# Optimization experiments

Hardware: AMD Instinct MI355X
Metric: run time of the kernel (lower is better)

## Reference

```python
import jax, jax.numpy as jnp
import numpy as np

TNEI = 2
TOPK = 4
NEIGH = 2 * TNEI + 1  # window size = 5


def _normalize(x, eps=1e-12):
    # matches torch F.normalize(dim=-1)
    n = jnp.linalg.norm(x, axis=-1, keepdims=True)
    return x / jnp.maximum(n, eps)


def setup_inputs() -> dict:
    key = jax.random.key(0)
    ks = jax.random.split(key, 10)
    B, T, C = 32, 256, 128
    x = jax.random.normal(ks[0], (B, T, C), jnp.float32)
    radj = jax.random.randint(ks[1], (B, T, T), 0, 2).astype(jnp.int32)
    inxs = jax.random.randint(ks[2], (B, T, TOPK), 0, T)
    s = 1.0 / np.sqrt(C)
    W_pf = jax.random.normal(ks[3], (C, C), jnp.float32) * s
    W_ns = jax.random.normal(ks[4], (C, C), jnp.float32) * s
    W_v = jax.random.normal(ks[5], (C, C), jnp.float32) * s
    v_pf = jax.random.normal(ks[6], (NEIGH,), jnp.float32)
    g_pf = jnp.linalg.norm(v_pf)[None]  # weight_norm gain, shape (1,)
    v_ns = jax.random.normal(ks[7], (TOPK,), jnp.float32)
    g_ns = jnp.linalg.norm(v_ns)[None]
    return dict(x=x, radj=radj, inxs=inxs, W_pf=W_pf, W_ns=W_ns, W_v=W_v,
                v_pf=v_pf, g_pf=g_pf, v_ns=v_ns, g_ns=g_ns)


def reference(x, radj, inxs, W_pf, W_ns, W_v, v_pf, g_pf, v_ns, g_ns):
    B, T, C = x.shape
    pf = _normalize(x @ W_pf.T)
    ns = _normalize(x @ W_ns.T)
    v = x @ W_v.T
    # windowed neighbor indices, identical to _tneigh_mask(mode='all')
    i = jnp.arange(T)
    start = jnp.clip(i - TNEI, 0, T - NEIGH)
    nbr = start[:, None] + jnp.arange(NEIGH)[None, :]  # (T, NEIGH)
    ctx = pf[:, nbr]  # (B, T, NEIGH, C) — replaces one-hot ctxinx einsum
    # pairwise window similarity: (B,T,T,n,n)
    sim = jnp.einsum('bxic,byjc->bxyij', ctx, ctx)
    # AdaptiveMaxPool2d((n,1)) == max over the last (key-window) axis
    sim_pf = sim.max(axis=-1)  # (B,T,T,n)
    w_pf = g_pf[0] * v_pf / jnp.linalg.norm(v_pf)  # weight-norm agg_pf
    sim_pf = jnp.einsum('bxyi,i->bxy', sim_pf, w_pf)
    # topk-neighbor branch: inxs gathers ns rows (replaces one-hot einsum)
    ns_q = ns[jnp.arange(B)[:, None, None], inxs]  # (B,T,TOPK,C)
    sim_ns = jnp.einsum('bxnc,byc->bxyn', ns_q, ns)  # (B,T,T,TOPK)
    w_ns = g_ns[0] * v_ns / jnp.linalg.norm(v_ns)  # weight-norm agg_ns
    sim_ns = jnp.einsum('bxyn,n->bxy', sim_ns, w_ns)
    # adjacency mask: 0 -> -1e22, >0 -> 0
    mask = jnp.where(radj == 0, jnp.float32(-1e22), jnp.float32(0.0))
    attn = jax.nn.softmax(sim_pf + sim_ns + mask, axis=-1)  # (B,T,T)
    return jnp.einsum('bkt,btd->bkd', attn, v)  # (B,T,C)
```

## Files before the change

### kernel.cpp

```cpp
#include <hip/hip_runtime.h>
#include <math.h>


#define TT 256
#define CC 128

using bf16x8 = __attribute__((ext_vector_type(8))) short;
using f32x4  = __attribute__((ext_vector_type(4))) float;

__device__ __forceinline__ short bf_hi(float x) {
    unsigned u = __float_as_uint(x);
    return (short)((u + 0x7FFFu + ((u >> 16) & 1u)) >> 16);
}
__device__ __forceinline__ void bf_split(float x, short& h, short& l) {
    h = bf_hi(x);
    float hf = __uint_as_float(((unsigned)(unsigned short)h) << 16);
    l = bf_hi(x - hf);
}
__device__ __forceinline__ float max5(float a, float b, float c, float d, float e) {
    return fmaxf(fmaxf(fmaxf(a, b), fmaxf(c, d)), e);
}

__global__ __launch_bounds__(256) void proj_kernel(
    const float* __restrict__ x,
    const float* __restrict__ W0, const float* __restrict__ W1, const float* __restrict__ W2,
    short* __restrict__ pf_h, short* __restrict__ pf_l,
    short* __restrict__ ns_h, short* __restrict__ ns_l,
    float* __restrict__ ns_f, float* __restrict__ v_f)
{
    __shared__ float xs[64][36];
    __shared__ float Ws[128][36];
    const int tid = threadIdx.x, ty = tid >> 4, tx = tid & 15;
    const int row0 = blockIdx.x * 64;
    const int m = blockIdx.y;
    const float* __restrict__ W = (m == 0) ? W0 : (m == 1) ? W1 : W2;
    float acc[4][8] = {};

    for (int k0 = 0; k0 < CC; k0 += 32) {
        __syncthreads();
        for (int i = 0; i < 2; i++) {
            int flat = i * 256 + tid, r = flat >> 3, q = (flat & 7) * 4;
            *(float4*)&xs[r][q] = *(const float4*)&x[(row0 + r) * CC + k0 + q];
        }
        for (int i = 0; i < 4; i++) {
            int flat = i * 256 + tid, r = flat >> 3, q = (flat & 7) * 4;
            *(float4*)&Ws[r][q] = *(const float4*)&W[r * CC + k0 + q];
        }
        __syncthreads();
        for (int kq = 0; kq < 32; kq += 4) {
            float4 av[4], bv[8];
            for (int u = 0; u < 4; u++) av[u] = *(float4*)&xs[ty + 16 * u][kq];
            for (int w = 0; w < 8; w++) bv[w] = *(float4*)&Ws[tx + 16 * w][kq];
            for (int u = 0; u < 4; u++)
                for (int w = 0; w < 8; w++) {
                    acc[u][w] = fmaf(av[u].x, bv[w].x, acc[u][w]);
                    acc[u][w] = fmaf(av[u].y, bv[w].y, acc[u][w]);
                    acc[u][w] = fmaf(av[u].z, bv[w].z, acc[u][w]);
                    acc[u][w] = fmaf(av[u].w, bv[w].w, acc[u][w]);
                }
        }
    }
    for (int u = 0; u < 4; u++) {
        int row = row0 + ty + 16 * u;
        if (m == 2) {
            for (int w = 0; w < 8; w++) v_f[row * CC + tx + 16 * w] = acc[u][w];
        } else {
            float ss = 0.f;
            for (int w = 0; w < 8; w++) ss += acc[u][w] * acc[u][w];
            for (int off = 8; off; off >>= 1) ss += __shfl_xor(ss, off);
            float inv = 1.f / fmaxf(sqrtf(ss), 1e-12f);
            for (int w = 0; w < 8; w++) {
                float v = acc[u][w] * inv;
                short h, l;
                bf_split(v, h, l);
                int idx = row * CC + tx + 16 * w;
                if (m == 0) { pf_h[idx] = h; pf_l[idx] = l; }
                else        { ns_h[idx] = h; ns_l[idx] = l; ns_f[idx] = v; }
            }
        }
    }
}

__global__ __launch_bounds__(256) void prep_kernel(
    const float* __restrict__ ns_f, const int* __restrict__ inxs,
    const float* __restrict__ v_ns, const float* __restrict__ g_ns,
    const float* __restrict__ v_f,
    short* __restrict__ q_h, short* __restrict__ q_l,
    short* __restrict__ vt_h, short* __restrict__ vt_l)
{
    __shared__ float Ls[64][132];
    const int bx = blockIdx.x, tid = threadIdx.x;
    if (bx < 512) {
        float n2 = v_ns[0]*v_ns[0] + v_ns[1]*v_ns[1] + v_ns[2]*v_ns[2] + v_ns[3]*v_ns[3];
        float sc = g_ns[0] / sqrtf(n2);
        const float w0 = sc*v_ns[0], w1 = sc*v_ns[1], w2 = sc*v_ns[2], w3 = sc*v_ns[3];
        for (int it = 0; it < 2; it++) {
            int t4 = bx * 512 + it * 256 + tid;
            int q = (t4 & 31) * 4, gr = t4 >> 5;
            int b = gr >> 8;
            int4 id = *(const int4*)&inxs[gr * 4];
            const float* Nb = ns_f + (size_t)b * TT * CC;
            float4 aa = *(const float4*)&Nb[id.x * CC + q];
            float4 ab = *(const float4*)&Nb[id.y * CC + q];
            float4 ac = *(const float4*)&Nb[id.z * CC + q];
            float4 ad = *(const float4*)&Nb[id.w * CC + q];
            float4 r4;
            r4.x = w0*aa.x + w1*ab.x + w2*ac.x + w3*ad.x;
            r4.y = w0*aa.y + w1*ab.y + w2*ac.y + w3*ad.y;
            r4.z = w0*aa.z + w1*ab.z + w2*ac.z + w3*ad.z;
            r4.w = w0*aa.w + w1*ab.w + w2*ac.w + w3*ad.w;
            short4 h4, l4;
            bf_split(r4.x, h4.x, l4.x); bf_split(r4.y, h4.y, l4.y);
            bf_split(r4.z, h4.z, l4.z); bf_split(r4.w, h4.w, l4.w);
            *(short4*)&q_h[(size_t)gr * CC + q] = h4;
            *(short4*)&q_l[(size_t)gr * CC + q] = l4;
        }
    } else {
        int blk = bx - 512;
        int b = blk >> 2, t0 = (blk & 3) * 64;
        const float* Vb = v_f + (size_t)b * TT * CC;
        for (int i = 0; i < 8; i++) {
            int flat = i * 256 + tid, r = flat >> 5, cq = (flat & 31) * 4;
            *(float4*)&Ls[r][cq] = *(const float4*)&Vb[(t0 + r) * CC + cq];
        }
        __syncthreads();
        int c = tid & 127, th = tid >> 7;
        for (int j = 0; j < 8; j++) {
            short4 h4, l4;
            for (int e = 0; e < 4; e++) {
                float v = Ls[th * 32 + j * 4 + e][c];
                bf_split(v, ((short*)&h4)[e], ((short*)&l4)[e]);
            }
            size_t o = ((size_t)b * CC + c) * TT + t0 + th * 32 + j * 4;
            *(short4*)&vt_h[o] = h4;
            *(short4*)&vt_l[o] = l4;
        }
    }
}

__global__ __launch_bounds__(256) void gram_mfma(
    const short* __restrict__ pf_h, const short* __restrict__ pf_l,
    const short* __restrict__ ns_h, const short* __restrict__ ns_l,
    const short* __restrict__ q_h,  const short* __restrict__ q_l,
    float* __restrict__ G, float* __restrict__ S)
{
    const int tid = threadIdx.x;
    const int m0 = blockIdx.x * 64, n0 = blockIdx.y * 64;
    const int b = blockIdx.z >> 1, half = blockIdx.z & 1;
    const size_t base = (size_t)b * TT * CC;
    const short* __restrict__ Ahp = (half ? q_h : pf_h) + base;
    const short* __restrict__ Alp = (half ? q_l : pf_l) + base;
    const short* __restrict__ Bhp = (half ? ns_h : pf_h) + base;
    const short* __restrict__ Blp = (half ? ns_l : pf_l) + base;
    const int lane = tid & 63, wave = tid >> 6;
    const int wm = wave >> 1, wn = wave & 1;
    const int quad = lane >> 4, lr = lane & 15;
    const int am0 = (m0 + 32 * wm + lr) * CC, am1 = am0 + 16 * CC;
    const int bn0 = (n0 + 32 * wn + lr) * CC, bn1 = bn0 + 16 * CC;
    f32x4 z4 = {0.f, 0.f, 0.f, 0.f};
    f32x4 acc[2][2] = {{z4, z4}, {z4, z4}};
    #pragma unroll
    for (int k0 = 0; k0 < CC; k0 += 32) {
        int ko = k0 + quad * 8;
        bf16x8 a0h = *(const bf16x8*)&Ahp[am0 + ko];
        bf16x8 a0l = *(const bf16x8*)&Alp[am0 + ko];
        bf16x8 a1h = *(const bf16x8*)&Ahp[am1 + ko];
        bf16x8 a1l = *(const bf16x8*)&Alp[am1 + ko];
        bf16x8 b0h = *(const bf16x8*)&Bhp[bn0 + ko];
        bf16x8 b0l = *(const bf16x8*)&Blp[bn0 + ko];
        bf16x8 b1h = *(const bf16x8*)&Bhp[bn1 + ko];
        bf16x8 b1l = *(const bf16x8*)&Blp[bn1 + ko];
        acc[0][0] = __builtin_amdgcn_mfma_f32_16x16x32_bf16(a0h, b0h, acc[0][0], 0, 0, 0);
        acc[0][0] = __builtin_amdgcn_mfma_f32_16x16x32_bf16(a0h, b0l, acc[0][0], 0, 0, 0);
        acc[0][0] = __builtin_amdgcn_mfma_f32_16x16x32_bf16(a0l, b0h, acc[0][0], 0, 0, 0);
        acc[0][1] = __builtin_amdgcn_mfma_f32_16x16x32_bf16(a0h, b1h, acc[0][1], 0, 0, 0);
        acc[0][1] = __builtin_amdgcn_mfma_f32_16x16x32_bf16(a0h, b1l, acc[0][1], 0, 0, 0);
        acc[0][1] = __builtin_amdgcn_mfma_f32_16x16x32_bf16(a0l, b1h, acc[0][1], 0, 0, 0);
        acc[1][0] = __builtin_amdgcn_mfma_f32_16x16x32_bf16(a1h, b0h, acc[1][0], 0, 0, 0);
        acc[1][0] = __builtin_amdgcn_mfma_f32_16x16x32_bf16(a1h, b0l, acc[1][0], 0, 0, 0);
        acc[1][0] = __builtin_amdgcn_mfma_f32_16x16x32_bf16(a1l, b0h, acc[1][0], 0, 0, 0);
        acc[1][1] = __builtin_amdgcn_mfma_f32_16x16x32_bf16(a1h, b1h, acc[1][1], 0, 0, 0);
        acc[1][1] = __builtin_amdgcn_mfma_f32_16x16x32_bf16(a1h, b1l, acc[1][1], 0, 0, 0);
        acc[1][1] = __builtin_amdgcn_mfma_f32_16x16x32_bf16(a1l, b1h, acc[1][1], 0, 0, 0);
    }
    float* __restrict__ Cb = (half ? S : G) + (size_t)b * TT * TT;
    for (int tm = 0; tm < 2; tm++)
        for (int tn = 0; tn < 2; tn++) {
            int rb = m0 + 32 * wm + 16 * tm + quad * 4;
            int cb = n0 + 32 * wn + 16 * tn + lr;
            for (int reg = 0; reg < 4; reg++)
                Cb[(size_t)(rb + reg) * TT + cb] = acc[tm][tn][reg];
        }
}

__global__ __launch_bounds__(256, 2) void fused_smax_pv(
    const float* __restrict__ G, const float* __restrict__ S,
    const int* __restrict__ radj, const float* __restrict__ v_pf,
    const float* __restrict__ g_pf,
    const short* __restrict__ vt_h, const short* __restrict__ vt_l,
    float* __restrict__ out)
{
    __shared__ float Gs[20 * 256];
    __shared__ float RM[20 * 256];
    __shared__ short ATH[16 * 264];
    __shared__ short ATL[16 * 264];
    __shared__ float RD[64];
    __shared__ float RMX[64];
    const int tid = threadIdx.x;
    const int xt = blockIdx.x, b = blockIdx.y;
    const int x0 = xt * 16;
    const int rbase = min(max(x0 - 2, 0), TT - 5);
    for (int i = 0; i < 5; i++) {
        int flat = i * 256 + tid, ri = flat >> 6, q = (flat & 63) * 4;
        int r = min(rbase + ri, TT - 1);
        *(float4*)&Gs[ri * 256 + q] = *(const float4*)&G[(size_t)b * TT * TT + r * TT + q];
    }
    float n2 = 0.f;
    for (int i = 0; i < 5; i++) n2 += v_pf[i] * v_pf[i];
    float sc = g_pf[0] / sqrtf(n2);
    float wpf[5];
    for (int i = 0; i < 5; i++) wpf[i] = sc * v_pf[i];
    __syncthreads();
    for (int t = 0; t < 5; t++) {
        int task = t * 256 + tid;
        int i = task >> 6, g = task & 63;
        const float* row = &Gs[i * 256];
        float4 X = *(float4*)&row[4 * g];
        float m0_, m1_, m2_, m3_;
        if (g == 0) {
            float4 N = *(float4*)&row[4];
            float mx = fmaxf(fmaxf(X.x, X.y), fmaxf(X.z, X.w));
            m0_ = m1_ = m2_ = fmaxf(mx, N.x);
            m3_ = max5(X.y, X.z, X.w, N.x, N.y);
        } else if (g == 63) {
            float4 P = *(float4*)&row[248];
            m0_ = max5(P.z, P.w, X.x, X.y, X.z);
            float mx = fmaxf(fmaxf(X.x, X.y), fmaxf(X.z, X.w));
            m1_ = m2_ = m3_ = fmaxf(P.w, mx);
        } else {
            float4 P = *(float4*)&row[4 * g - 4];
            float4 N = *(float4*)&row[4 * g + 4];
            m0_ = max5(P.z, P.w, X.x, X.y, X.z);
            m1_ = max5(P.w, X.x, X.y, X.z, X.w);
            m2_ = max5(X.x, X.y, X.z, X.w, N.x);
            m3_ = max5(X.y, X.z, X.w, N.x, N.y);
        }
        float4 o4 = {m0_, m1_, m2_, m3_};
        *(float4*)&RM[i * 256 + 4 * g] = o4;
    }
    __syncthreads();
    const int y = tid;
    const size_t sb = (size_t)b * TT * TT;
    float lv[16];
    if (xt > 0 && xt < 15) {
        float rm[20];
        #pragma unroll
        for (int r = 0; r < 20; r++) rm[r] = RM[r * 256 + y];
        #pragma unroll
        for (int xi = 0; xi < 16; xi++) {
            float s = wpf[0] * rm[xi];
            #pragma unroll
            for (int i = 1; i < 5; i++) s = fmaf(wpf[i], rm[xi + i], s);
            lv[xi] = s;
        }
    } else {
        for (int xi = 0; xi < 16; xi++) {
            int sxr = min(max(x0 + xi - 2, 0), TT - 5) - rbase;
            float s = 0.f;
            for (int i = 0; i < 5; i++) s = fmaf(wpf[i], RM[(sxr + i) * 256 + y], s);
            lv[xi] = s;
        }
    }
    for (int xi = 0; xi < 16; xi++) {
        lv[xi] += S[sb + (x0 + xi) * TT + y];
        if (radj[sb + (x0 + xi) * TT + y] == 0) lv[xi] += -1e22f;
    }
    const int lane = tid & 63, wv = tid >> 6;
    for (int xi = 0; xi < 16; xi++) {
        float v = lv[xi];
        for (int o = 32; o; o >>= 1) v = fmaxf(v, __shfl_xor(v, o));
        if (lane == 0) RMX[xi * 4 + wv] = v;
    }
    __syncthreads();
    for (int xi = 0; xi < 16; xi++) {
        float mx = fmaxf(fmaxf(RMX[xi * 4], RMX[xi * 4 + 1]),
                         fmaxf(RMX[xi * 4 + 2], RMX[xi * 4 + 3]));
        float e = __expf(lv[xi] - mx);
        short h, l;
        bf_split(e, h, l);
        ATH[xi * 264 + y] = h;
        ATL[xi * 264 + y] = l;
        for (int o = 32; o; o >>= 1) e += __shfl_xor(e, o);
        if (lane == 0) RD[xi * 4 + wv] = e;
    }
    __syncthreads();
    const int quad = lane >> 4, lr = lane & 15;
    const int c0 = wv * 32;
    const short* __restrict__ vhb = vt_h + (size_t)b * CC * TT;
    const short* __restrict__ vlb = vt_l + (size_t)b * CC * TT;
    const int ar0 = (c0 + lr) * TT, ar1 = ar0 + 16 * TT;
    f32x4 z4 = {0.f, 0.f, 0.f, 0.f};
    f32x4 acc[2] = {z4, z4};
    #pragma unroll
    for (int k0 = 0; k0 < TT; k0 += 32) {
        int ko = k0 + quad * 8;
        bf16x8 bh = *(bf16x8*)&ATH[lr * 264 + ko];
        bf16x8 bl = *(bf16x8*)&ATL[lr * 264 + ko];
        bf16x8 a0h = *(const bf16x8*)&vhb[ar0 + ko];
        bf16x8 a0l = *(const bf16x8*)&vlb[ar0 + ko];
        bf16x8 a1h = *(const bf16x8*)&vhb[ar1 + ko];
        bf16x8 a1l = *(const bf16x8*)&vlb[ar1 + ko];
        acc[0] = __builtin_amdgcn_mfma_f32_16x16x32_bf16(a0h, bh, acc[0], 0, 0, 0);
        acc[0] = __builtin_amdgcn_mfma_f32_16x16x32_bf16(a0h, bl, acc[0], 0, 0, 0);
        acc[0] = __builtin_amdgcn_mfma_f32_16x16x32_bf16(a0l, bh, acc[0], 0, 0, 0);
        acc[1] = __builtin_amdgcn_mfma_f32_16x16x32_bf16(a1h, bh, acc[1], 0, 0, 0);
        acc[1] = __builtin_amdgcn_mfma_f32_16x16x32_bf16(a1h, bl, acc[1], 0, 0, 0);
        acc[1] = __builtin_amdgcn_mfma_f32_16x16x32_bf16(a1l, bh, acc[1], 0, 0, 0);
    }
    float sm = RD[lr * 4] + RD[lr * 4 + 1] + RD[lr * 4 + 2] + RD[lr * 4 + 3];
    float rinv = 1.f / sm;
    for (int tm = 0; tm < 2; tm++) {
        float4 r;
        r.x = acc[tm][0] * rinv; r.y = acc[tm][1] * rinv;
        r.z = acc[tm][2] * rinv; r.w = acc[tm][3] * rinv;
        *(float4*)&out[(size_t)b * TT * CC + (x0 + lr) * CC + c0 + 16 * tm + quad * 4] = r;
    }
}

extern "C" void kernel_launch(void* const* d_in, const int* in_sizes, int n_in,
                              void* d_out, int out_size, void* d_ws, size_t ws_size,
                              hipStream_t stream) {
    const float* x    = (const float*)d_in[0];
    const int*   radj = (const int*)d_in[1];
    const int*   inxs = (const int*)d_in[2];
    const float* Wpf  = (const float*)d_in[3];
    const float* Wns  = (const float*)d_in[4];
    const float* Wv   = (const float*)d_in[5];
    const float* v_pf = (const float*)d_in[6];
    const float* g_pf = (const float*)d_in[7];
    const float* v_ns = (const float*)d_in[8];
    const float* g_ns = (const float*)d_in[9];
    float* out = (float*)d_out;

    char* base = (char*)d_ws;
    float* ns_f = (float*)(base);
    float* v_f  = (float*)(base + (4u << 20));
    short* pf_h = (short*)(base + (8u << 20));
    short* pf_l = (short*)(base + (10u << 20));
    short* ns_h = (short*)(base + (12u << 20));
    short* ns_l = (short*)(base + (14u << 20));
    short* q_h  = (short*)(base + (16u << 20));
    short* q_l  = (short*)(base + (18u << 20));
    short* vt_h = (short*)(base + (20u << 20));
    short* vt_l = (short*)(base + (22u << 20));
    float* G    = (float*)(base + (24u << 20));
    float* S    = (float*)(base + (32u << 20));

    proj_kernel<<<dim3(128, 3), 256, 0, stream>>>(x, Wpf, Wns, Wv,
                                                  pf_h, pf_l, ns_h, ns_l, ns_f, v_f);
    prep_kernel<<<640, 256, 0, stream>>>(ns_f, inxs, v_ns, g_ns, v_f,
                                         q_h, q_l, vt_h, vt_l);
    gram_mfma<<<dim3(4, 4, 64), 256, 0, stream>>>(pf_h, pf_l, ns_h, ns_l, q_h, q_l, G, S);
    fused_smax_pv<<<dim3(16, 32), 256, 0, stream>>>(G, S, radj, v_pf, g_pf,
                                                    vt_h, vt_l, out);
}
```

Baseline: 144.5 us.

## Fuse prep into projection and gram kernels, use split-bf16 MFMA projections

The projection GEMM moves from scalar FP32 FMAs to split-bf16 (hi/lo) MFMA on 32-row tiles, and writes the transposed split V directly from the accumulators. The separate prep kernel is removed: the top-k weighted gather of ns rows now happens inside the gram kernel's shared-memory tile load, which also does the bf16 splitting on the fly from FP32 pf/ns. This removes one kernel launch and the intermediate hi/lo buffers. In exchange, the gram kernel does redundant gather and split work across column tiles, with extra LDS traffic and barriers.

```diff
diff --git a/kernel.cpp b/kernel.cpp
--- a/kernel.cpp
+++ b/kernel.cpp
@@ -21,167 +21,175 @@
     return fmaxf(fmaxf(fmaxf(a, b), fmaxf(c, d)), e);
 }
 
-__global__ __launch_bounds__(256) void proj_kernel(
+__global__ __launch_bounds__(256, 4) void proj_kernel(
     const float* __restrict__ x,
     const float* __restrict__ W0, const float* __restrict__ W1, const float* __restrict__ W2,
-    short* __restrict__ pf_h, short* __restrict__ pf_l,
-    short* __restrict__ ns_h, short* __restrict__ ns_l,
-    float* __restrict__ ns_f, float* __restrict__ v_f)
+    float* __restrict__ pf, float* __restrict__ ns,
+    short* __restrict__ vt_h, short* __restrict__ vt_l)
 {
-    __shared__ float xs[64][36];
-    __shared__ float Ws[128][36];
-    const int tid = threadIdx.x, ty = tid >> 4, tx = tid & 15;
-    const int row0 = blockIdx.x * 64;
+    __shared__ short Ah[32 * 40], Al[32 * 40];
+    __shared__ short Bh[128 * 40], Bl[128 * 40];
+    __shared__ float ssb[32][4];
+    const int tid = threadIdx.x;
+    const int row0 = blockIdx.x * 32;
     const int m = blockIdx.y;
     const float* __restrict__ W = (m == 0) ? W0 : (m == 1) ? W1 : W2;
-    float acc[4][8] = {};
+    const int lane = tid & 63, wn = tid >> 6;
+    const int quad = lane >> 4, lr = lane & 15;
+    f32x4 z4 = {0.f, 0.f, 0.f, 0.f};
+    f32x4 acc[2][2] = {{z4, z4}, {z4, z4}};
 
     for (int k0 = 0; k0 < CC; k0 += 32) {
         __syncthreads();
-        for (int i = 0; i < 2; i++) {
-            int flat = i * 256 + tid, r = flat >> 3, q = (flat & 7) * 4;
-            *(float4*)&xs[r][q] = *(const float4*)&x[(row0 + r) * CC + k0 + q];
+        {
+            int r = tid >> 3, q = (tid & 7) * 4;
+            float4 a4 = *(const float4*)&x[(row0 + r) * CC + k0 + q];
+            short4 h4, l4;
+            bf_split(a4.x, h4.x, l4.x); bf_split(a4.y, h4.y, l4.y);
+            bf_split(a4.z, h4.z, l4.z); bf_split(a4.w, h4.w, l4.w);
+            *(short4*)&Ah[r * 40 + q] = h4; *(short4*)&Al[r * 40 + q] = l4;
         }
         for (int i = 0; i < 4; i++) {
             int flat = i * 256 + tid, r = flat >> 3, q = (flat & 7) * 4;
-            *(float4*)&Ws[r][q] = *(const float4*)&W[r * CC + k0 + q];
-        }
-        __syncthreads();
-        for (int kq = 0; kq < 32; kq += 4) {
-            float4 av[4], bv[8];
-            for (int u = 0; u < 4; u++) av[u] = *(float4*)&xs[ty + 16 * u][kq];
-            for (int w = 0; w < 8; w++) bv[w] = *(float4*)&Ws[tx + 16 * w][kq];
-            for (int u = 0; u < 4; u++)
-                for (int w = 0; w < 8; w++) {
-                    acc[u][w] = fmaf(av[u].x, bv[w].x, acc[u][w]);
-                    acc[u][w] = fmaf(av[u].y, bv[w].y, acc[u][w]);
-                    acc[u][w] = fmaf(av[u].z, bv[w].z, acc[u][w]);
-                    acc[u][w] = fmaf(av[u].w, bv[w].w, acc[u][w]);
-                }
-        }
-    }
-    for (int u = 0; u < 4; u++) {
-        int row = row0 + ty + 16 * u;
-        if (m == 2) {
-            for (int w = 0; w < 8; w++) v_f[row * CC + tx + 16 * w] = acc[u][w];
-        } else {
-            float ss = 0.f;
-            for (int w = 0; w < 8; w++) ss += acc[u][w] * acc[u][w];
-            for (int off = 8; off; off >>= 1) ss += __shfl_xor(ss, off);
-            float inv = 1.f / fmaxf(sqrtf(ss), 1e-12f);
-            for (int w = 0; w < 8; w++) {
-                float v = acc[u][w] * inv;
-                short h, l;
-                bf_split(v, h, l);
-                int idx = row * CC + tx + 16 * w;
-                if (m == 0) { pf_h[idx] = h; pf_l[idx] = l; }
-                else        { ns_h[idx] = h; ns_l[idx] = l; ns_f[idx] = v; }
-            }
-        }
-    }
-}
-
-__global__ __launch_bounds__(256) void prep_kernel(
-    const float* __restrict__ ns_f, const int* __restrict__ inxs,
-    const float* __restrict__ v_ns, const float* __restrict__ g_ns,
-    const float* __restrict__ v_f,
-    short* __restrict__ q_h, short* __restrict__ q_l,
-    short* __restrict__ vt_h, short* __restrict__ vt_l)
+            float4 b4 = *(const float4*)&W[r * CC + k0 + q];
+            short4 h4, l4;
+            bf_split(b4.x, h4.x, l4.x); bf_split(b4.y, h4.y, l4.y);
+            bf_split(b4.z, h4.z, l4.z); bf_split(b4.w, h4.w, l4.w);
+            *(short4*)&Bh[r * 40 + q] = h4; *(short4*)&Bl[r * 40 + q] = l4;
+        }
+        __syncthreads();
+        bf16x8 ah[2], al[2], bh[2], bl[2];
+        for (int ra = 0; ra < 2; ra++) {
+            int ar = (16 * ra + lr) * 40 + quad * 8;
+            ah[ra] = *(bf16x8*)&Ah[ar];
+            al[ra] = *(bf16x8*)&Al[ar];
+        }
+        for (int tn = 0; tn < 2; tn++) {
+            int br = (32 * wn + 16 * tn + lr) * 40 + quad * 8;
+            bh[tn] = *(bf16x8*)&Bh[br];
+            bl[tn] = *(bf16x8*)&Bl[br];
+        }
+        for (int ra = 0; ra < 2; ra++)
+            for (int tn = 0; tn < 2; tn++) {
+                acc[ra][tn] = __builtin_amdgcn_mfma_f32_16x16x32_bf16(ah[ra], bh[tn], acc[ra][tn], 0, 0, 0);
+                acc[ra][tn] = __builtin_amdgcn_mfma_f32_16x16x32_bf16(ah[ra], bl[tn], acc[ra][tn], 0, 0, 0);
+                acc[ra][tn] = __builtin_amdgcn_mfma_f32_16x16x32_bf16(al[ra], bh[tn], acc[ra][tn], 0, 0, 0);
+            }
+    }
+    if (m < 2) {
+        float* __restrict__ o = (m == 0) ? pf : ns;
+        float ssp[2][4];
+        for (int ra = 0; ra < 2; ra++)
+            for (int reg = 0; reg < 4; reg++) {
+                float s = acc[ra][0][reg] * acc[ra][0][reg]
+                        + acc[ra][1][reg] * acc[ra][1][reg];
+                for (int off = 1; off < 16; off <<= 1) s += __shfl_xor(s, off);
+                ssp[ra][reg] = s;
+            }
+        if (lr == 0)
+            for (int ra = 0; ra < 2; ra++)
+                for (int reg = 0; reg < 4; reg++)
+                    ssb[16 * ra + quad * 4 + reg][wn] = ssp[ra][reg];
+        __syncthreads();
+        for (int ra = 0; ra < 2; ra++)
+            for (int reg = 0; reg < 4; reg++) {
+                int ml = 16 * ra + quad * 4 + reg;
+                float ss = ssb[ml][0] + ssb[ml][1] + ssb[ml][2] + ssb[ml][3];
+                float inv = 1.f / fmaxf(sqrtf(ss), 1e-12f);
+                int row = row0 + ml;
+                for (int tn = 0; tn < 2; tn++)
+                    o[row * CC + 32 * wn + 16 * tn + lr] = acc[ra][tn][reg] * inv;
+            }
+    } else {
+        for (int ra = 0; ra < 2; ra++) {
+            int rowbase = row0 + 16 * ra + quad * 4;
+            int b = rowbase >> 8, t0 = rowbase & 255;
+            for (int tn = 0; tn < 2; tn++) {
+                int c = 32 * wn + 16 * tn + lr;
+                short4 h4, l4;
+                for (int reg = 0; reg < 4; reg++)
+                    bf_split(acc[ra][tn][reg], ((short*)&h4)[reg], ((short*)&l4)[reg]);
+                size_t o = ((size_t)b * CC + c) * TT + t0;
+                *(short4*)&vt_h[o] = h4;
+                *(short4*)&vt_l[o] = l4;
+            }
+        }
+    }
+}
+
+__global__ __launch_bounds__(256, 4) void gram_mfma(
+    const float* __restrict__ pf, const float* __restrict__ ns,
+    const int* __restrict__ inxs, const float* __restrict__ v_ns,
+    const float* __restrict__ g_ns, float* __restrict__ G, float* __restrict__ S)
 {
-    __shared__ float Ls[64][132];
-    const int bx = blockIdx.x, tid = threadIdx.x;
-    if (bx < 512) {
-        float n2 = v_ns[0]*v_ns[0] + v_ns[1]*v_ns[1] + v_ns[2]*v_ns[2] + v_ns[3]*v_ns[3];
-        float sc = g_ns[0] / sqrtf(n2);
-        const float w0 = sc*v_ns[0], w1 = sc*v_ns[1], w2 = sc*v_ns[2], w3 = sc*v_ns[3];
-        for (int it = 0; it < 2; it++) {
-            int t4 = bx * 512 + it * 256 + tid;
-            int q = (t4 & 31) * 4, gr = t4 >> 5;
-            int b = gr >> 8;
-            int4 id = *(const int4*)&inxs[gr * 4];
-            const float* Nb = ns_f + (size_t)b * TT * CC;
-            float4 aa = *(const float4*)&Nb[id.x * CC + q];
-            float4 ab = *(const float4*)&Nb[id.y * CC + q];
-            float4 ac = *(const float4*)&Nb[id.z * CC + q];
-            float4 ad = *(const float4*)&Nb[id.w * CC + q];
-            float4 r4;
-            r4.x = w0*aa.x + w1*ab.x + w2*ac.x + w3*ad.x;
-            r4.y = w0*aa.y + w1*ab.y + w2*ac.y + w3*ad.y;
-            r4.z = w0*aa.z + w1*ab.z + w2*ac.z + w3*ad.z;
-            r4.w = w0*aa.w + w1*ab.w + w2*ac.w + w3*ad.w;
-            short4 h4, l4;
-            bf_split(r4.x, h4.x, l4.x); bf_split(r4.y, h4.y, l4.y);
-            bf_split(r4.z, h4.z, l4.z); bf_split(r4.w, h4.w, l4.w);
-            *(short4*)&q_h[(size_t)gr * CC + q] = h4;
-            *(short4*)&q_l[(size_t)gr * CC + q] = l4;
-        }
-    } else {
-        int blk = bx - 512;
-        int b = blk >> 2, t0 = (blk & 3) * 64;
-        const float* Vb = v_f + (size_t)b * TT * CC;
-        for (int i = 0; i < 8; i++) {
-            int flat = i * 256 + tid, r = flat >> 5, cq = (flat & 31) * 4;
-            *(float4*)&Ls[r][cq] = *(const float4*)&Vb[(t0 + r) * CC + cq];
-        }
-        __syncthreads();
-        int c = tid & 127, th = tid >> 7;
-        for (int j = 0; j < 8; j++) {
-            short4 h4, l4;
-            for (int e = 0; e < 4; e++) {
-                float v = Ls[th * 32 + j * 4 + e][c];
-                bf_split(v, ((short*)&h4)[e], ((short*)&l4)[e]);
-            }
-            size_t o = ((size_t)b * CC + c) * TT + t0 + th * 32 + j * 4;
-            *(short4*)&vt_h[o] = h4;
-            *(short4*)&vt_l[o] = l4;
-        }
-    }
-}
-
-__global__ __launch_bounds__(256) void gram_mfma(
-    const short* __restrict__ pf_h, const short* __restrict__ pf_l,
-    const short* __restrict__ ns_h, const short* __restrict__ ns_l,
-    const short* __restrict__ q_h,  const short* __restrict__ q_l,
-    float* __restrict__ G, float* __restrict__ S)
-{
+    __shared__ short Ah[64 * 40], Al[64 * 40], Bh[64 * 40], Bl[64 * 40];
     const int tid = threadIdx.x;
     const int m0 = blockIdx.x * 64, n0 = blockIdx.y * 64;
     const int b = blockIdx.z >> 1, half = blockIdx.z & 1;
-    const size_t base = (size_t)b * TT * CC;
-    const short* __restrict__ Ahp = (half ? q_h : pf_h) + base;
-    const short* __restrict__ Alp = (half ? q_l : pf_l) + base;
-    const short* __restrict__ Bhp = (half ? ns_h : pf_h) + base;
-    const short* __restrict__ Blp = (half ? ns_l : pf_l) + base;
+    const float* __restrict__ Pb = pf + (size_t)b * TT * CC;
+    const float* __restrict__ Nb = ns + (size_t)b * TT * CC;
+    const float* __restrict__ Bsrc = half ? Nb : Pb;
+
+    float w0 = 0.f, w1 = 0.f, w2 = 0.f, w3 = 0.f;
+    int4 id0 = {0, 0, 0, 0}, id1 = {0, 0, 0, 0};
+    if (half) {
+        float n2 = v_ns[0]*v_ns[0] + v_ns[1]*v_ns[1] + v_ns[2]*v_ns[2] + v_ns[3]*v_ns[3];
+        float sc = g_ns[0] / sqrtf(n2);
+        w0 = sc*v_ns[0]; w1 = sc*v_ns[1]; w2 = sc*v_ns[2]; w3 = sc*v_ns[3];
+        id0 = *(const int4*)&inxs[(b * TT + m0 + (tid >> 3)) * 4];
+        id1 = *(const int4*)&inxs[(b * TT + m0 + 32 + (tid >> 3)) * 4];
+    }
+
     const int lane = tid & 63, wave = tid >> 6;
     const int wm = wave >> 1, wn = wave & 1;
     const int quad = lane >> 4, lr = lane & 15;
-    const int am0 = (m0 + 32 * wm + lr) * CC, am1 = am0 + 16 * CC;
-    const int bn0 = (n0 + 32 * wn + lr) * CC, bn1 = bn0 + 16 * CC;
     f32x4 z4 = {0.f, 0.f, 0.f, 0.f};
     f32x4 acc[2][2] = {{z4, z4}, {z4, z4}};
-    #pragma unroll
+
     for (int k0 = 0; k0 < CC; k0 += 32) {
-        int ko = k0 + quad * 8;
-        bf16x8 a0h = *(const bf16x8*)&Ahp[am0 + ko];
-        bf16x8 a0l = *(const bf16x8*)&Alp[am0 + ko];
-        bf16x8 a1h = *(const bf16x8*)&Ahp[am1 + ko];
-        bf16x8 a1l = *(const bf16x8*)&Alp[am1 + ko];
-        bf16x8 b0h = *(const bf16x8*)&Bhp[bn0 + ko];
-        bf16x8 b0l = *(const bf16x8*)&Blp[bn0 + ko];
-        bf16x8 b1h = *(const bf16x8*)&Bhp[bn1 + ko];
-        bf16x8 b1l = *(const bf16x8*)&Blp[bn1 + ko];
-        acc[0][0] = __builtin_amdgcn_mfma_f32_16x16x32_bf16(a0h, b0h, acc[0][0], 0, 0, 0);
-        acc[0][0] = __builtin_amdgcn_mfma_f32_16x16x32_bf16(a0h, b0l, acc[0][0], 0, 0, 0);
-        acc[0][0] = __builtin_amdgcn_mfma_f32_16x16x32_bf16(a0l, b0h, acc[0][0], 0, 0, 0);
-        acc[0][1] = __builtin_amdgcn_mfma_f32_16x16x32_bf16(a0h, b1h, acc[0][1], 0, 0, 0);
-        acc[0][1] = __builtin_amdgcn_mfma_f32_16x16x32_bf16(a0h, b1l, acc[0][1], 0, 0, 0);
-        acc[0][1] = __builtin_amdgcn_mfma_f32_16x16x32_bf16(a0l, b1h, acc[0][1], 0, 0, 0);
-        acc[1][0] = __builtin_amdgcn_mfma_f32_16x16x32_bf16(a1h, b0h, acc[1][0], 0, 0, 0);
-        acc[1][0] = __builtin_amdgcn_mfma_f32_16x16x32_bf16(a1h, b0l, acc[1][0], 0, 0, 0);
-        acc[1][0] = __builtin_amdgcn_mfma_f32_16x16x32_bf16(a1l, b0h, acc[1][0], 0, 0, 0);
-        acc[1][1] = __builtin_amdgcn_mfma_f32_16x16x32_bf16(a1h, b1h, acc[1][1], 0, 0, 0);
-        acc[1][1] = __builtin_amdgcn_mfma_f32_16x16x32_bf16(a1h, b1l, acc[1][1], 0, 0, 0);
-        acc[1][1] = __builtin_amdgcn_mfma_f32_16x16x32_bf16(a1l, b1h, acc[1][1], 0, 0, 0);
+        __syncthreads();
+        for (int i = 0; i < 2; i++) {
+            int flat = i * 256 + tid, r = flat >> 3, q = (flat & 7) * 4;
+            float4 a4;
+            if (!half) {
+                a4 = *(const float4*)&Pb[(m0 + r) * CC + k0 + q];
+            } else {
+                int4 id = i ? id1 : id0;
+                float4 aa = *(const float4*)&Nb[id.x * CC + k0 + q];
+                float4 ab = *(const float4*)&Nb[id.y * CC + k0 + q];
+                float4 ac = *(const float4*)&Nb[id.z * CC + k0 + q];
+                float4 ad = *(const float4*)&Nb[id.w * CC + k0 + q];
+                a4.x = w0*aa.x + w1*ab.x + w2*ac.x + w3*ad.x;
+                a4.y = w0*aa.y + w1*ab.y + w2*ac.y + w3*ad.y;
+                a4.z = w0*aa.z + w1*ab.z + w2*ac.z + w3*ad.z;
+                a4.w = w0*aa.w + w1*ab.w + w2*ac.w + w3*ad.w;
+            }
+            float4 b4 = *(const float4*)&Bsrc[(n0 + r) * CC + k0 + q];
+            short4 h4, l4;
+            bf_split(a4.x, h4.x, l4.x); bf_split(a4.y, h4.y, l4.y);
+            bf_split(a4.z, h4.z, l4.z); bf_split(a4.w, h4.w, l4.w);
+            *(short4*)&Ah[r * 40 + q] = h4; *(short4*)&Al[r * 40 + q] = l4;
+            bf_split(b4.x, h4.x, l4.x); bf_split(b4.y, h4.y, l4.y);
+            bf_split(b4.z, h4.z, l4.z); bf_split(b4.w, h4.w, l4.w);
+            *(short4*)&Bh[r * 40 + q] = h4; *(short4*)&Bl[r * 40 + q] = l4;
+        }
+        __syncthreads();
+        bf16x8 bh[2], bl[2];
+        for (int tn = 0; tn < 2; tn++) {
+            int br = (32 * wn + 16 * tn + lr) * 40 + quad * 8;
+            bh[tn] = *(bf16x8*)&Bh[br];
+            bl[tn] = *(bf16x8*)&Bl[br];
+        }
+        for (int tm = 0; tm < 2; tm++) {
+            int ar = (32 * wm + 16 * tm + lr) * 40 + quad * 8;
+            bf16x8 ah = *(bf16x8*)&Ah[ar];
+            bf16x8 al = *(bf16x8*)&Al[ar];
+            for (int tn = 0; tn < 2; tn++) {
+                acc[tm][tn] = __builtin_amdgcn_mfma_f32_16x16x32_bf16(ah, bh[tn], acc[tm][tn], 0, 0, 0);
+                acc[tm][tn] = __builtin_amdgcn_mfma_f32_16x16x32_bf16(ah, bl[tn], acc[tm][tn], 0, 0, 0);
+                acc[tm][tn] = __builtin_amdgcn_mfma_f32_16x16x32_bf16(al, bh[tn], acc[tm][tn], 0, 0, 0);
+            }
+        }
     }
     float* __restrict__ Cb = (half ? S : G) + (size_t)b * TT * TT;
     for (int tm = 0; tm < 2; tm++)
@@ -343,24 +351,15 @@
     float* out = (float*)d_out;
 
     char* base = (char*)d_ws;
-    float* ns_f = (float*)(base);
-    float* v_f  = (float*)(base + (4u << 20));
-    short* pf_h = (short*)(base + (8u << 20));
-    short* pf_l = (short*)(base + (10u << 20));
-    short* ns_h = (short*)(base + (12u << 20));
-    short* ns_l = (short*)(base + (14u << 20));
-    short* q_h  = (short*)(base + (16u << 20));
-    short* q_l  = (short*)(base + (18u << 20));
-    short* vt_h = (short*)(base + (20u << 20));
-    short* vt_l = (short*)(base + (22u << 20));
-    float* G    = (float*)(base + (24u << 20));
-    float* S    = (float*)(base + (32u << 20));
-
-    proj_kernel<<<dim3(128, 3), 256, 0, stream>>>(x, Wpf, Wns, Wv,
-                                                  pf_h, pf_l, ns_h, ns_l, ns_f, v_f);
-    prep_kernel<<<640, 256, 0, stream>>>(ns_f, inxs, v_ns, g_ns, v_f,
-                                         q_h, q_l, vt_h, vt_l);
-    gram_mfma<<<dim3(4, 4, 64), 256, 0, stream>>>(pf_h, pf_l, ns_h, ns_l, q_h, q_l, G, S);
+    float* pf   = (float*)(base);
+    float* ns   = (float*)(base + (4u << 20));
+    short* vt_h = (short*)(base + (8u << 20));
+    short* vt_l = (short*)(base + (10u << 20));
+    float* G    = (float*)(base + (12u << 20));
+    float* S    = (float*)(base + (20u << 20));
+
+    proj_kernel<<<dim3(256, 3), 256, 0, stream>>>(x, Wpf, Wns, Wv, pf, ns, vt_h, vt_l);
+    gram_mfma<<<dim3(4, 4, 64), 256, 0, stream>>>(pf, ns, inxs, v_ns, g_ns, G, S);
     fused_smax_pv<<<dim3(16, 32), 256, 0, stream>>>(G, S, radj, v_pf, g_pf,
                                                     vt_h, vt_l, out);
 }
```

After: 126.6 us. 1.14x faster.
